# Kernel optimization log

Hardware: AMD Instinct MI355X
Metric: run time of the kernel (lower is better)

Reference implementation:

```python
import jax, jax.numpy as jnp
import numpy as np

ALPHA = 10.0
BETA = 2.0
BASE = 0.5
N, D, N_CLASSES = 4096, 512, 128


def setup_inputs() -> dict:
    key = jax.random.key(0)
    k1, k2 = jax.random.split(key)
    x = jax.random.normal(k1, (N, D), dtype=jnp.float32)
    inputs = x / jnp.linalg.norm(x, axis=1, keepdims=True)  # L2-normalized embeddings
    targets = jax.random.randint(k2, (N,), 0, N_CLASSES, dtype=jnp.int64)
    margin = jnp.float32(0.5)
    return {"inputs": inputs, "targets": targets, "margin": margin}


def reference(inputs, targets, margin):
    # Vectorized equivalent of the per-row masked_select/sort/hard-mining loop.
    n = inputs.shape[0]
    sim = inputs @ inputs.T  # [n, n]
    same = targets[:, None] == targets[None, :]
    pos_mask = same & (sim < 1.0)        # positives, excluding self-sim == 1
    neg_mask = ~same

    # sort()[0] / sort()[-1]  ==  masked min / max
    min_pos = jnp.min(jnp.where(pos_mask, sim, jnp.inf), axis=1)    # pos_pair_[0]
    max_neg = jnp.max(jnp.where(neg_mask, sim, -jnp.inf), axis=1)   # neg_pair_[-1]

    # Hard mining: selected values equal the raw sims (the +/- margin and
    # min_pos/max_neg shifts cancel algebraically in the original code).
    sel_neg = neg_mask & (sim + margin - min_pos[:, None] > 0)
    sel_pos = pos_mask & (max_neg[:, None] - sim + margin > 0)

    pos_sum = jnp.sum(jnp.where(sel_pos, jnp.exp(-BETA * (sim - BASE)), 0.0), axis=1)
    neg_sum = jnp.sum(jnp.where(sel_neg, jnp.exp(ALPHA * (sim - BASE)), 0.0), axis=1)
    row_loss = (2.0 / BETA) * jnp.log1p(pos_sum) + (2.0 / ALPHA) * jnp.log1p(neg_sum)

    # Rows with no surviving pos or neg pairs are skipped (counted in c).
    valid = jnp.any(sel_pos, axis=1) & jnp.any(sel_neg, axis=1)
    loss = jnp.sum(jnp.where(valid, row_loss, 0.0)) / n
    prec = jnp.mean((~valid).astype(jnp.float32))

    # Original returns mean sims of the LAST row's (pre-mining) pos/neg pairs.
    lp = pos_mask[-1].astype(sim.dtype)
    ln = neg_mask[-1].astype(sim.dtype)
    mean_pos_sim = jnp.sum(sim[-1] * lp) / jnp.maximum(jnp.sum(lp), 1.0)
    mean_neg_sim = jnp.sum(sim[-1] * ln) / jnp.maximum(jnp.sum(ln), 1.0)
    return (loss, prec, mean_pos_sim, mean_neg_sim)
```

## Files before the change

kernel.cpp:

```cpp
#include <hip/hip_runtime.h>
#include <hip/hip_bf16.h>
#include <math.h>

#define NROWS 4096
#define DDIM  512
#define BM    128
#define BK    64
#define NT    (DDIM / BK)
#define NBLK  (NROWS / BM)
#define NTRI  (NBLK * (NBLK + 1) / 2)

static constexpr float ALPHA = 10.0f;
static constexpr float BETA  = 2.0f;
static constexpr float BASE  = 0.5f;

typedef short bf16x8 __attribute__((ext_vector_type(8)));
typedef float f32x4 __attribute__((ext_vector_type(4)));

__device__ __forceinline__ unsigned enc_f32(float f) {
  unsigned b = __float_as_uint(f);
  return (b & 0x80000000u) ? ~b : (b | 0x80000000u);
}
__device__ __forceinline__ float dec_f32(unsigned u) {
  unsigned b = (u & 0x80000000u) ? (u & 0x7fffffffu) : ~u;
  return __uint_as_float(b);
}
__device__ __forceinline__ unsigned f2bf(float f) {
  __hip_bfloat16 h = __float2bfloat16(f);
  return (unsigned)*reinterpret_cast<unsigned short*>(&h);
}
__device__ __forceinline__ float bf2f(unsigned short u) {
  return __uint_as_float(((unsigned)u) << 16);
}

#define GLOAD_LDS16(g, l)                                              \
  __builtin_amdgcn_global_load_lds(                                    \
      (const __attribute__((address_space(1))) void*)(g),              \
      (__attribute__((address_space(3))) void*)(l), 16, 0, 0)

__global__ __launch_bounds__(256) void convert_k(
    const float* __restrict__ X, unsigned short* __restrict__ Xb,
    float* __restrict__ selfsim, unsigned* __restrict__ minb,
    unsigned* __restrict__ maxb, float* __restrict__ lacc) {
  const int gid = blockIdx.x * 256 + threadIdx.x;
  if (gid < NROWS) {
    minb[gid] = 0xFF800000u;
    maxb[gid] = 0x007FFFFFu;
  }
  if (gid < 8) lacc[gid] = 0.0f;

  const int wid = threadIdx.x >> 6, lane = threadIdx.x & 63;
  const int r = blockIdx.x * 4 + wid;
  const size_t base = (size_t)r * DDIM + lane * 8;
  const float4 v0 = *reinterpret_cast<const float4*>(X + base);
  const float4 v1 = *reinterpret_cast<const float4*>(X + base + 4);
  uint4 u;
  u.x = f2bf(v0.x) | (f2bf(v0.y) << 16);
  u.y = f2bf(v0.z) | (f2bf(v0.w) << 16);
  u.z = f2bf(v1.x) | (f2bf(v1.y) << 16);
  u.w = f2bf(v1.z) | (f2bf(v1.w) << 16);
  *reinterpret_cast<uint4*>(Xb + base) = u;

  float sd = v0.x * v0.x;
  sd = fmaf(v0.y, v0.y, sd); sd = fmaf(v0.z, v0.z, sd); sd = fmaf(v0.w, v0.w, sd);
  sd = fmaf(v1.x, v1.x, sd); sd = fmaf(v1.y, v1.y, sd);
  sd = fmaf(v1.z, v1.z, sd); sd = fmaf(v1.w, v1.w, sd);
  #pragma unroll
  for (int off = 1; off < 64; off <<= 1) sd += __shfl_xor(sd, off);
  if (lane == 0) selfsim[r] = sd;
}

__global__ __launch_bounds__(256) void gemm_tri(
    const unsigned short* __restrict__ Xb, const int* __restrict__ tgt,
    const float* __restrict__ selfsim,
    unsigned* __restrict__ minb, unsigned* __restrict__ maxb,
    unsigned short* __restrict__ simb) {
  __shared__ unsigned short lds[2][2][BM * BK] __attribute__((aligned(16)));

  int kk0 = blockIdx.x, bi = 0;
  while (kk0 >= NBLK - bi) { kk0 -= NBLK - bi; ++bi; }
  const int bj = bi + kk0;
  const int i0 = bi * BM, j0 = bj * BM;
  const bool diagb = (bi == bj);

  const int tid = threadIdx.x;
  const int w = tid >> 6, lane = tid & 63;
  const int wr = w >> 1, wc = w & 1;
  const int g = lane >> 4, q = lane & 15;
  const char* Xbb = (const char*)Xb;

  f32x4 acc[4][4];
  #pragma unroll
  for (int m = 0; m < 4; ++m)
    #pragma unroll
    for (int n = 0; n < 4; ++n) acc[m][n] = (f32x4)0.0f;

  #define STAGE(buf, t)                                                          \
    do {                                                                         \
      const int kb_ = (t) * (BK * 2);                                            \
      _Pragma("unroll")                                                          \
      for (int c_ = 0; c_ < 4; ++c_) {                                           \
        const int lin_ = (c_ * 256 + tid) * 16;                                  \
        const int row_ = lin_ >> 7;                                              \
        const int col_ = lin_ & 127;                                             \
        const int scol_ = col_ ^ ((row_ & 7) << 4);                              \
        GLOAD_LDS16(Xbb + (size_t)(i0 + row_) * (DDIM * 2) + kb_ + scol_,        \
                    (char*)&lds[buf][0][0] + lin_);                              \
        GLOAD_LDS16(Xbb + (size_t)(j0 + row_) * (DDIM * 2) + kb_ + scol_,        \
                    (char*)&lds[buf][1][0] + lin_);                              \
      }                                                                          \
    } while (0)

  STAGE(0, 0);
  __syncthreads();
  int cur = 0;
  for (int t = 0; t < NT; ++t) {
    if (t + 1 < NT) STAGE(cur ^ 1, t + 1);
    const char* Ab = (const char*)&lds[cur][0][0];
    const char* Bb = (const char*)&lds[cur][1][0];
    #pragma unroll
    for (int kk = 0; kk < 2; ++kk) {
      bf16x8 a[4], b[4];
      #pragma unroll
      for (int fm = 0; fm < 4; ++fm) {
        const int row = wr * 64 + fm * 16 + q;
        const int col = (kk * 64 + g * 16) ^ ((row & 7) << 4);
        a[fm] = *reinterpret_cast<const bf16x8*>(Ab + row * 128 + col);
      }
      #pragma unroll
      for (int fn = 0; fn < 4; ++fn) {
        const int row = wc * 64 + fn * 16 + q;
        const int col = (kk * 64 + g * 16) ^ ((row & 7) << 4);
        b[fn] = *reinterpret_cast<const bf16x8*>(Bb + row * 128 + col);
      }
      #pragma unroll
      for (int fm = 0; fm < 4; ++fm)
        #pragma unroll
        for (int fn = 0; fn < 4; ++fn)
          acc[fm][fn] = __builtin_amdgcn_mfma_f32_16x16x32_bf16(a[fm], b[fn], acc[fm][fn], 0, 0, 0);
    }
    __syncthreads();
    cur ^= 1;
  }

  const int rbase = i0 + wr * 64;
  int cg[4], tj[4];
  #pragma unroll
  for (int fn = 0; fn < 4; ++fn) {
    cg[fn] = j0 + wc * 64 + fn * 16 + q;
    tj[fn] = tgt[cg[fn]];
  }
  int ti[16];
  #pragma unroll
  for (int fm = 0; fm < 4; ++fm)
    #pragma unroll
    for (int reg = 0; reg < 4; ++reg)
      ti[fm * 4 + reg] = tgt[rbase + fm * 16 + g * 4 + reg];

  #pragma unroll
  for (int fm = 0; fm < 4; ++fm) {
    #pragma unroll
    for (int reg = 0; reg < 4; ++reg) {
      const int r = rbase + fm * 16 + g * 4 + reg;
      const int tr = ti[fm * 4 + reg];
      float mnp = INFINITY, mxn = -INFINITY;
      #pragma unroll
      for (int fn = 0; fn < 4; ++fn) {
        float s = acc[fm][fn][reg];
        if (diagb && r == cg[fn]) s = selfsim[r];
        simb[(size_t)r * NROWS + cg[fn]] = (unsigned short)f2bf(s);
        if (tj[fn] == tr) {
          if (s < 1.0f) mnp = fminf(mnp, s);
        } else {
          mxn = fmaxf(mxn, s);
        }
      }
      #pragma unroll
      for (int off = 1; off < 16; off <<= 1) {
        mnp = fminf(mnp, __shfl_xor(mnp, off));
        mxn = fmaxf(mxn, __shfl_xor(mxn, off));
      }
      if (q == 0) {
        atomicMin(minb + r, enc_f32(mnp));
        atomicMax(maxb + r, enc_f32(mxn));
      }
    }
  }

  if (!diagb) {
    #pragma unroll
    for (int fn = 0; fn < 4; ++fn) {
      const int c = cg[fn];
      const int tc = tj[fn];
      float mnp = INFINITY, mxn = -INFINITY;
      #pragma unroll
      for (int fm = 0; fm < 4; ++fm)
        #pragma unroll
        for (int reg = 0; reg < 4; ++reg) {
          const float s = acc[fm][fn][reg];
          if (ti[fm * 4 + reg] == tc) {
            if (s < 1.0f) mnp = fminf(mnp, s);
          } else {
            mxn = fmaxf(mxn, s);
          }
        }
      mnp = fminf(mnp, __shfl_xor(mnp, 16));
      mnp = fminf(mnp, __shfl_xor(mnp, 32));
      mxn = fmaxf(mxn, __shfl_xor(mxn, 16));
      mxn = fmaxf(mxn, __shfl_xor(mxn, 32));
      if (lane < 16) {
        atomicMin(minb + c, enc_f32(mnp));
        atomicMax(maxb + c, enc_f32(mxn));
      }
    }
    #pragma unroll
    for (int fm = 0; fm < 4; ++fm)
      #pragma unroll
      for (int fn = 0; fn < 4; ++fn) {
        uint2 uu;
        uu.x = f2bf(acc[fm][fn][0]) | (f2bf(acc[fm][fn][1]) << 16);
        uu.y = f2bf(acc[fm][fn][2]) | (f2bf(acc[fm][fn][3]) << 16);
        *reinterpret_cast<uint2*>(simb + (size_t)cg[fn] * NROWS + rbase + fm * 16 + g * 4) = uu;
      }
  }
}

__global__ __launch_bounds__(256) void row_pass(
    const unsigned short* __restrict__ simb, const int* __restrict__ tgt,
    const unsigned* __restrict__ minb, const unsigned* __restrict__ maxb,
    float* __restrict__ rowloss, float* __restrict__ rowvalid,
    float* __restrict__ lacc, const float* __restrict__ marginp) {
  const int wid = threadIdx.x >> 6, lane = threadIdx.x & 63;
  const int i = blockIdx.x * 4 + wid;
  const int ti = tgt[i];
  const float mp = dec_f32(minb[i]);
  const float mx = dec_f32(maxb[i]);
  const float margin = *marginp;
  const unsigned short* row = simb + (size_t)i * NROWS;
  const bool last = (i == NROWS - 1);

  float psum = 0.0f, nsum = 0.0f, lsp = 0.0f, lcp = 0.0f, lsn = 0.0f, lcn = 0.0f;
  #pragma unroll
  for (int c = 0; c < 8; ++c) {
    const int j0 = c * 512 + lane * 8;
    const bf16x8 v = *reinterpret_cast<const bf16x8*>(row + j0);
    const int4 t0 = *reinterpret_cast<const int4*>(tgt + j0);
    const int4 t1 = *reinterpret_cast<const int4*>(tgt + j0 + 4);
    const int tj[8] = {t0.x, t0.y, t0.z, t0.w, t1.x, t1.y, t1.z, t1.w};
    #pragma unroll
    for (int e = 0; e < 8; ++e) {
      const float s = bf2f((unsigned short)v[e]);
      if (tj[e] != ti) {
        if (s + margin - mp > 0.0f) nsum += __expf(ALPHA * (s - BASE));
        if (last) { lsn += s; lcn += 1.0f; }
      } else if (s < 1.0f) {
        if (mx - s + margin > 0.0f) psum += __expf(-BETA * (s - BASE));
        if (last) { lsp += s; lcp += 1.0f; }
      }
    }
  }
  #pragma unroll
  for (int off = 1; off < 64; off <<= 1) {
    psum += __shfl_xor(psum, off);
    nsum += __shfl_xor(nsum, off);
  }
  if (last) {
    #pragma unroll
    for (int off = 1; off < 64; off <<= 1) {
      lsp += __shfl_xor(lsp, off); lcp += __shfl_xor(lcp, off);
      lsn += __shfl_xor(lsn, off); lcn += __shfl_xor(lcn, off);
    }
  }
  if (lane == 0) {
    const bool valid = (psum > 0.0f) && (nsum > 0.0f);
    rowloss[i] = valid ? (2.0f / BETA) * log1pf(psum) + (2.0f / ALPHA) * log1pf(nsum) : 0.0f;
    rowvalid[i] = valid ? 0.0f : 1.0f;
    if (last) { lacc[0] = lsp; lacc[1] = lcp; lacc[2] = lsn; lacc[3] = lcn; }
  }
}

__device__ __forceinline__ float block_sum(float v) {
  __shared__ float sh[4];
  #pragma unroll
  for (int off = 32; off > 0; off >>= 1) v += __shfl_down(v, off);
  if ((threadIdx.x & 63) == 0) sh[threadIdx.x >> 6] = v;
  __syncthreads();
  float r = sh[0] + sh[1] + sh[2] + sh[3];
  __syncthreads();
  return r;
}

__global__ __launch_bounds__(256) void finalize_k(
    const float* __restrict__ rowloss, const float* __restrict__ rowvalid,
    const float* __restrict__ lacc, float* __restrict__ out) {
  float lsum = 0.0f, inval = 0.0f;
  #pragma unroll
  for (int c = 0; c < 16; ++c) {
    const int i = c * 256 + threadIdx.x;
    lsum += rowloss[i];
    inval += rowvalid[i];
  }
  lsum = block_sum(lsum);
  inval = block_sum(inval);
  if (threadIdx.x == 0) {
    out[0] = lsum / (float)NROWS;
    out[1] = inval / (float)NROWS;
    out[2] = lacc[0] / fmaxf(lacc[1], 1.0f);
    out[3] = lacc[2] / fmaxf(lacc[3], 1.0f);
  }
}

extern "C" void kernel_launch(void* const* d_in, const int* in_sizes, int n_in,
                              void* d_out, int out_size, void* d_ws, size_t ws_size,
                              hipStream_t stream) {
  const float* X = (const float*)d_in[0];
  const int* tgt = (const int*)d_in[1];
  const float* marginp = (const float*)d_in[2];
  float* out = (float*)d_out;

  char* ws = (char*)d_ws;
  unsigned* minb = (unsigned*)ws;
  unsigned* maxb = (unsigned*)(ws + (16 << 10));
  float* rowloss = (float*)(ws + (32 << 10));
  float* rowvalid = (float*)(ws + (48 << 10));
  float* lacc = (float*)(ws + (64 << 10));
  float* selfsim = (float*)(ws + (80 << 10));
  unsigned short* Xb = (unsigned short*)(ws + (128 << 10));
  unsigned short* simb = (unsigned short*)(ws + (128 << 10) + ((size_t)4 << 20));

  convert_k<<<dim3(NROWS / 4), 256, 0, stream>>>(X, Xb, selfsim, minb, maxb, lacc);
  gemm_tri<<<dim3(NTRI), 256, 0, stream>>>(Xb, tgt, selfsim, minb, maxb, simb);
  row_pass<<<dim3(NROWS / 4), 256, 0, stream>>>(simb, tgt, minb, maxb, rowloss, rowvalid, lacc, marginp);
  finalize_k<<<dim3(1), 256, 0, stream>>>(rowloss, rowvalid, lacc, out);
}
```

Before: 124.8 us.

## Recompute similarity GEMM in second pass instead of materializing bf16 sim matrix

Drops the 4096x4096 bf16 similarity buffer and the row_pass kernel that re-read it. The triangular GEMM now runs twice: the first pass computes per-row min-positive and max-negative, and the second recomputes the tile and accumulates the masked exp sums per row and column with atomics. Diagonal blocks load only one tile, and atomics are skipped when a lane holds the identity value. This trades a 32 MB write plus read of the sim matrix for a second pass of GEMM compute and more float atomics, which also makes the summation order nondeterministic.

```diff
diff --git a/kernel.cpp b/kernel.cpp
--- a/kernel.cpp
+++ b/kernel.cpp
@@ -38,14 +38,17 @@
       (const __attribute__((address_space(1))) void*)(g),              \
       (__attribute__((address_space(3))) void*)(l), 16, 0, 0)
 
-__global__ __launch_bounds__(256) void convert_k(
+__global__ __launch_bounds__(256) void convert_init_k(
     const float* __restrict__ X, unsigned short* __restrict__ Xb,
     float* __restrict__ selfsim, unsigned* __restrict__ minb,
-    unsigned* __restrict__ maxb, float* __restrict__ lacc) {
+    unsigned* __restrict__ maxb, float* __restrict__ ps,
+    float* __restrict__ ns, float* __restrict__ lacc) {
   const int gid = blockIdx.x * 256 + threadIdx.x;
   if (gid < NROWS) {
     minb[gid] = 0xFF800000u;
     maxb[gid] = 0x007FFFFFu;
+    ps[gid] = 0.0f;
+    ns[gid] = 0.0f;
   }
   if (gid < 8) lacc[gid] = 0.0f;
 
@@ -70,11 +73,27 @@
   if (lane == 0) selfsim[r] = sd;
 }
 
-__global__ __launch_bounds__(256) void gemm_tri(
+#define STAGE1(dst, rowbase, t)                                                \
+  do {                                                                         \
+    const int kb_ = (t) * (BK * 2);                                            \
+    _Pragma("unroll")                                                          \
+    for (int c_ = 0; c_ < 4; ++c_) {                                           \
+      const int lin_ = (c_ * 256 + tid) * 16;                                  \
+      const int row_ = lin_ >> 7;                                              \
+      const int col_ = lin_ & 127;                                             \
+      const int scol_ = col_ ^ ((row_ & 7) << 4);                              \
+      GLOAD_LDS16(Xbb + (size_t)((rowbase) + row_) * (DDIM * 2) + kb_ + scol_, \
+                  (char*)(dst) + lin_);                                        \
+    }                                                                          \
+  } while (0)
+
+template <int PASS>
+__global__ __launch_bounds__(256) void gemm_pass(
     const unsigned short* __restrict__ Xb, const int* __restrict__ tgt,
     const float* __restrict__ selfsim,
     unsigned* __restrict__ minb, unsigned* __restrict__ maxb,
-    unsigned short* __restrict__ simb) {
+    float* __restrict__ ps, float* __restrict__ ns,
+    float* __restrict__ lacc, const float* __restrict__ marginp) {
   __shared__ unsigned short lds[2][2][BM * BK] __attribute__((aligned(16)));
 
   int kk0 = blockIdx.x, bi = 0;
@@ -95,29 +114,17 @@
     #pragma unroll
     for (int n = 0; n < 4; ++n) acc[m][n] = (f32x4)0.0f;
 
-  #define STAGE(buf, t)                                                          \
-    do {                                                                         \
-      const int kb_ = (t) * (BK * 2);                                            \
-      _Pragma("unroll")                                                          \
-      for (int c_ = 0; c_ < 4; ++c_) {                                           \
-        const int lin_ = (c_ * 256 + tid) * 16;                                  \
-        const int row_ = lin_ >> 7;                                              \
-        const int col_ = lin_ & 127;                                             \
-        const int scol_ = col_ ^ ((row_ & 7) << 4);                              \
-        GLOAD_LDS16(Xbb + (size_t)(i0 + row_) * (DDIM * 2) + kb_ + scol_,        \
-                    (char*)&lds[buf][0][0] + lin_);                              \
-        GLOAD_LDS16(Xbb + (size_t)(j0 + row_) * (DDIM * 2) + kb_ + scol_,        \
-                    (char*)&lds[buf][1][0] + lin_);                              \
-      }                                                                          \
-    } while (0)
-
-  STAGE(0, 0);
+  STAGE1(&lds[0][0][0], i0, 0);
+  if (!diagb) STAGE1(&lds[0][1][0], j0, 0);
   __syncthreads();
   int cur = 0;
   for (int t = 0; t < NT; ++t) {
-    if (t + 1 < NT) STAGE(cur ^ 1, t + 1);
+    if (t + 1 < NT) {
+      STAGE1(&lds[cur ^ 1][0][0], i0, t + 1);
+      if (!diagb) STAGE1(&lds[cur ^ 1][1][0], j0, t + 1);
+    }
     const char* Ab = (const char*)&lds[cur][0][0];
-    const char* Bb = (const char*)&lds[cur][1][0];
+    const char* Bb = diagb ? Ab : (const char*)&lds[cur][1][0];
     #pragma unroll
     for (int kk = 0; kk < 2; ++kk) {
       bf16x8 a[4], b[4];
@@ -157,125 +164,155 @@
     for (int reg = 0; reg < 4; ++reg)
       ti[fm * 4 + reg] = tgt[rbase + fm * 16 + g * 4 + reg];
 
-  #pragma unroll
-  for (int fm = 0; fm < 4; ++fm) {
-    #pragma unroll
-    for (int reg = 0; reg < 4; ++reg) {
-      const int r = rbase + fm * 16 + g * 4 + reg;
-      const int tr = ti[fm * 4 + reg];
-      float mnp = INFINITY, mxn = -INFINITY;
-      #pragma unroll
-      for (int fn = 0; fn < 4; ++fn) {
-        float s = acc[fm][fn][reg];
-        if (diagb && r == cg[fn]) s = selfsim[r];
-        simb[(size_t)r * NROWS + cg[fn]] = (unsigned short)f2bf(s);
-        if (tj[fn] == tr) {
-          if (s < 1.0f) mnp = fminf(mnp, s);
-        } else {
-          mxn = fmaxf(mxn, s);
-        }
-      }
-      #pragma unroll
-      for (int off = 1; off < 16; off <<= 1) {
-        mnp = fminf(mnp, __shfl_xor(mnp, off));
-        mxn = fmaxf(mxn, __shfl_xor(mxn, off));
-      }
-      if (q == 0) {
-        atomicMin(minb + r, enc_f32(mnp));
-        atomicMax(maxb + r, enc_f32(mxn));
-      }
-    }
-  }
-
-  if (!diagb) {
-    #pragma unroll
-    for (int fn = 0; fn < 4; ++fn) {
-      const int c = cg[fn];
-      const int tc = tj[fn];
-      float mnp = INFINITY, mxn = -INFINITY;
-      #pragma unroll
-      for (int fm = 0; fm < 4; ++fm)
-        #pragma unroll
-        for (int reg = 0; reg < 4; ++reg) {
-          const float s = acc[fm][fn][reg];
-          if (ti[fm * 4 + reg] == tc) {
+  if constexpr (PASS == 0) {
+    #pragma unroll
+    for (int fm = 0; fm < 4; ++fm) {
+      #pragma unroll
+      for (int reg = 0; reg < 4; ++reg) {
+        const int r = rbase + fm * 16 + g * 4 + reg;
+        const int tr = ti[fm * 4 + reg];
+        float mnp = INFINITY, mxn = -INFINITY;
+        #pragma unroll
+        for (int fn = 0; fn < 4; ++fn) {
+          float s = acc[fm][fn][reg];
+          if (diagb && r == cg[fn]) s = selfsim[r];
+          if (tj[fn] == tr) {
             if (s < 1.0f) mnp = fminf(mnp, s);
           } else {
             mxn = fmaxf(mxn, s);
           }
         }
-      mnp = fminf(mnp, __shfl_xor(mnp, 16));
-      mnp = fminf(mnp, __shfl_xor(mnp, 32));
-      mxn = fmaxf(mxn, __shfl_xor(mxn, 16));
-      mxn = fmaxf(mxn, __shfl_xor(mxn, 32));
-      if (lane < 16) {
-        atomicMin(minb + c, enc_f32(mnp));
-        atomicMax(maxb + c, enc_f32(mxn));
-      }
-    }
+        #pragma unroll
+        for (int off = 1; off < 16; off <<= 1) {
+          mnp = fminf(mnp, __shfl_xor(mnp, off));
+          mxn = fmaxf(mxn, __shfl_xor(mxn, off));
+        }
+        if (q == 0) {
+          if (mnp != INFINITY) atomicMin(minb + r, enc_f32(mnp));
+          if (mxn != -INFINITY) atomicMax(maxb + r, enc_f32(mxn));
+        }
+      }
+    }
+    if (!diagb) {
+      #pragma unroll
+      for (int fn = 0; fn < 4; ++fn) {
+        const int tc = tj[fn];
+        float mnp = INFINITY, mxn = -INFINITY;
+        #pragma unroll
+        for (int fm = 0; fm < 4; ++fm)
+          #pragma unroll
+          for (int reg = 0; reg < 4; ++reg) {
+            const float s = acc[fm][fn][reg];
+            if (ti[fm * 4 + reg] == tc) {
+              if (s < 1.0f) mnp = fminf(mnp, s);
+            } else {
+              mxn = fmaxf(mxn, s);
+            }
+          }
+        mnp = fminf(mnp, __shfl_xor(mnp, 16));
+        mnp = fminf(mnp, __shfl_xor(mnp, 32));
+        mxn = fmaxf(mxn, __shfl_xor(mxn, 16));
+        mxn = fmaxf(mxn, __shfl_xor(mxn, 32));
+        if (lane < 16) {
+          if (mnp != INFINITY) atomicMin(minb + cg[fn], enc_f32(mnp));
+          if (mxn != -INFINITY) atomicMax(maxb + cg[fn], enc_f32(mxn));
+        }
+      }
+    }
+  } else {
+    const float margin = *marginp;
+    float mpr[16], mxr[16];
     #pragma unroll
     for (int fm = 0; fm < 4; ++fm)
       #pragma unroll
+      for (int reg = 0; reg < 4; ++reg) {
+        const int r = rbase + fm * 16 + g * 4 + reg;
+        mpr[fm * 4 + reg] = dec_f32(minb[r]);
+        mxr[fm * 4 + reg] = dec_f32(maxb[r]);
+      }
+    float mpc[4], mxc[4], cps[4], cns[4];
+    #pragma unroll
+    for (int fn = 0; fn < 4; ++fn) {
+      mpc[fn] = dec_f32(minb[cg[fn]]);
+      mxc[fn] = dec_f32(maxb[cg[fn]]);
+      cps[fn] = 0.0f; cns[fn] = 0.0f;
+    }
+    float wlsp = 0, wlcp = 0, wlsn = 0, wlcn = 0;
+    float clsp = 0, clcp = 0, clsn = 0, clcn = 0;
+
+    #pragma unroll
+    for (int fm = 0; fm < 4; ++fm) {
+      #pragma unroll
+      for (int reg = 0; reg < 4; ++reg) {
+        const int idx = fm * 4 + reg;
+        const int r = rbase + fm * 16 + g * 4 + reg;
+        const int tr = ti[idx];
+        const bool lastrow = (r == NROWS - 1);
+        float rps = 0.0f, rns = 0.0f;
+        #pragma unroll
+        for (int fn = 0; fn < 4; ++fn) {
+          float s = acc[fm][fn][reg];
+          if (diagb && r == cg[fn])
+            s = bf2f((unsigned short)f2bf(selfsim[r]));
+          const bool collast = (!diagb) && (cg[fn] == NROWS - 1);
+          if (tj[fn] != tr) {
+            const float en = __expf(ALPHA * (s - BASE));
+            if (s + margin - mpr[idx] > 0.0f) rns += en;
+            if (!diagb && s + margin - mpc[fn] > 0.0f) cns[fn] += en;
+            if (lastrow) { wlsn += s; wlcn += 1.0f; }
+            if (collast) { clsn += s; clcn += 1.0f; }
+          } else if (s < 1.0f) {
+            const float ep = __expf(-BETA * (s - BASE));
+            if (mxr[idx] - s + margin > 0.0f) rps += ep;
+            if (!diagb && mxc[fn] - s + margin > 0.0f) cps[fn] += ep;
+            if (lastrow) { wlsp += s; wlcp += 1.0f; }
+            if (collast) { clsp += s; clcp += 1.0f; }
+          }
+        }
+        #pragma unroll
+        for (int off = 1; off < 16; off <<= 1) {
+          rps += __shfl_xor(rps, off);
+          rns += __shfl_xor(rns, off);
+        }
+        if (q == 0) {
+          if (rps != 0.0f) atomicAdd(ps + r, rps);
+          if (rns != 0.0f) atomicAdd(ns + r, rns);
+        }
+      }
+    }
+    if (bi == NBLK - 1 && wr == 1 && diagb) {
+      #pragma unroll
+      for (int off = 1; off < 16; off <<= 1) {
+        wlsp += __shfl_xor(wlsp, off); wlcp += __shfl_xor(wlcp, off);
+        wlsn += __shfl_xor(wlsn, off); wlcn += __shfl_xor(wlcn, off);
+      }
+      if (lane == 48) {
+        if (wlcp != 0.0f) { atomicAdd(lacc + 0, wlsp); atomicAdd(lacc + 1, wlcp); }
+        if (wlcn != 0.0f) { atomicAdd(lacc + 2, wlsn); atomicAdd(lacc + 3, wlcn); }
+      }
+    }
+    if (!diagb) {
+      #pragma unroll
       for (int fn = 0; fn < 4; ++fn) {
-        uint2 uu;
-        uu.x = f2bf(acc[fm][fn][0]) | (f2bf(acc[fm][fn][1]) << 16);
-        uu.y = f2bf(acc[fm][fn][2]) | (f2bf(acc[fm][fn][3]) << 16);
-        *reinterpret_cast<uint2*>(simb + (size_t)cg[fn] * NROWS + rbase + fm * 16 + g * 4) = uu;
-      }
-  }
-}
-
-__global__ __launch_bounds__(256) void row_pass(
-    const unsigned short* __restrict__ simb, const int* __restrict__ tgt,
-    const unsigned* __restrict__ minb, const unsigned* __restrict__ maxb,
-    float* __restrict__ rowloss, float* __restrict__ rowvalid,
-    float* __restrict__ lacc, const float* __restrict__ marginp) {
-  const int wid = threadIdx.x >> 6, lane = threadIdx.x & 63;
-  const int i = blockIdx.x * 4 + wid;
-  const int ti = tgt[i];
-  const float mp = dec_f32(minb[i]);
-  const float mx = dec_f32(maxb[i]);
-  const float margin = *marginp;
-  const unsigned short* row = simb + (size_t)i * NROWS;
-  const bool last = (i == NROWS - 1);
-
-  float psum = 0.0f, nsum = 0.0f, lsp = 0.0f, lcp = 0.0f, lsn = 0.0f, lcn = 0.0f;
-  #pragma unroll
-  for (int c = 0; c < 8; ++c) {
-    const int j0 = c * 512 + lane * 8;
-    const bf16x8 v = *reinterpret_cast<const bf16x8*>(row + j0);
-    const int4 t0 = *reinterpret_cast<const int4*>(tgt + j0);
-    const int4 t1 = *reinterpret_cast<const int4*>(tgt + j0 + 4);
-    const int tj[8] = {t0.x, t0.y, t0.z, t0.w, t1.x, t1.y, t1.z, t1.w};
-    #pragma unroll
-    for (int e = 0; e < 8; ++e) {
-      const float s = bf2f((unsigned short)v[e]);
-      if (tj[e] != ti) {
-        if (s + margin - mp > 0.0f) nsum += __expf(ALPHA * (s - BASE));
-        if (last) { lsn += s; lcn += 1.0f; }
-      } else if (s < 1.0f) {
-        if (mx - s + margin > 0.0f) psum += __expf(-BETA * (s - BASE));
-        if (last) { lsp += s; lcp += 1.0f; }
-      }
-    }
-  }
-  #pragma unroll
-  for (int off = 1; off < 64; off <<= 1) {
-    psum += __shfl_xor(psum, off);
-    nsum += __shfl_xor(nsum, off);
-  }
-  if (last) {
-    #pragma unroll
-    for (int off = 1; off < 64; off <<= 1) {
-      lsp += __shfl_xor(lsp, off); lcp += __shfl_xor(lcp, off);
-      lsn += __shfl_xor(lsn, off); lcn += __shfl_xor(lcn, off);
-    }
-  }
-  if (lane == 0) {
-    const bool valid = (psum > 0.0f) && (nsum > 0.0f);
-    rowloss[i] = valid ? (2.0f / BETA) * log1pf(psum) + (2.0f / ALPHA) * log1pf(nsum) : 0.0f;
-    rowvalid[i] = valid ? 0.0f : 1.0f;
-    if (last) { lacc[0] = lsp; lacc[1] = lcp; lacc[2] = lsn; lacc[3] = lcn; }
+        float v1 = cps[fn], v2 = cns[fn];
+        v1 += __shfl_xor(v1, 16); v1 += __shfl_xor(v1, 32);
+        v2 += __shfl_xor(v2, 16); v2 += __shfl_xor(v2, 32);
+        if (lane < 16) {
+          if (v1 != 0.0f) atomicAdd(ps + cg[fn], v1);
+          if (v2 != 0.0f) atomicAdd(ns + cg[fn], v2);
+        }
+      }
+      if (bj == NBLK - 1 && wc == 1) {
+        clsp += __shfl_xor(clsp, 16); clsp += __shfl_xor(clsp, 32);
+        clcp += __shfl_xor(clcp, 16); clcp += __shfl_xor(clcp, 32);
+        clsn += __shfl_xor(clsn, 16); clsn += __shfl_xor(clsn, 32);
+        clcn += __shfl_xor(clcn, 16); clcn += __shfl_xor(clcn, 32);
+        if (lane == 15) {
+          if (clcp != 0.0f) { atomicAdd(lacc + 0, clsp); atomicAdd(lacc + 1, clcp); }
+          if (clcn != 0.0f) { atomicAdd(lacc + 2, clsn); atomicAdd(lacc + 3, clcn); }
+        }
+      }
+    }
   }
 }
 
@@ -291,14 +328,18 @@
 }
 
 __global__ __launch_bounds__(256) void finalize_k(
-    const float* __restrict__ rowloss, const float* __restrict__ rowvalid,
+    const float* __restrict__ ps, const float* __restrict__ ns,
     const float* __restrict__ lacc, float* __restrict__ out) {
   float lsum = 0.0f, inval = 0.0f;
   #pragma unroll
   for (int c = 0; c < 16; ++c) {
     const int i = c * 256 + threadIdx.x;
-    lsum += rowloss[i];
-    inval += rowvalid[i];
+    const float p = ps[i], n = ns[i];
+    if (p > 0.0f && n > 0.0f) {
+      lsum += (2.0f / BETA) * log1pf(p) + (2.0f / ALPHA) * log1pf(n);
+    } else {
+      inval += 1.0f;
+    }
   }
   lsum = block_sum(lsum);
   inval = block_sum(inval);
@@ -321,15 +362,14 @@
   char* ws = (char*)d_ws;
   unsigned* minb = (unsigned*)ws;
   unsigned* maxb = (unsigned*)(ws + (16 << 10));
-  float* rowloss = (float*)(ws + (32 << 10));
-  float* rowvalid = (float*)(ws + (48 << 10));
+  float* ps = (float*)(ws + (32 << 10));
+  float* ns = (float*)(ws + (48 << 10));
   float* lacc = (float*)(ws + (64 << 10));
   float* selfsim = (float*)(ws + (80 << 10));
   unsigned short* Xb = (unsigned short*)(ws + (128 << 10));
-  unsigned short* simb = (unsigned short*)(ws + (128 << 10) + ((size_t)4 << 20));
-
-  convert_k<<<dim3(NROWS / 4), 256, 0, stream>>>(X, Xb, selfsim, minb, maxb, lacc);
-  gemm_tri<<<dim3(NTRI), 256, 0, stream>>>(Xb, tgt, selfsim, minb, maxb, simb);
-  row_pass<<<dim3(NROWS / 4), 256, 0, stream>>>(simb, tgt, minb, maxb, rowloss, rowvalid, lacc, marginp);
-  finalize_k<<<dim3(1), 256, 0, stream>>>(rowloss, rowvalid, lacc, out);
-}
+
+  convert_init_k<<<dim3(NROWS / 4), 256, 0, stream>>>(X, Xb, selfsim, minb, maxb, ps, ns, lacc);
+  gemm_pass<0><<<dim3(NTRI), 256, 0, stream>>>(Xb, tgt, selfsim, minb, maxb, ps, ns, lacc, marginp);
+  gemm_pass<1><<<dim3(NTRI), 256, 0, stream>>>(Xb, tgt, selfsim, minb, maxb, ps, ns, lacc, marginp);
+  finalize_k<<<dim3(1), 256, 0, stream>>>(ps, ns, lacc, out);
+}
```

New measurement: 153.3 us. 22.8% more time.

## Move min/max mining into row pass and stage sim tile stores through LDS

Applied to the files above, without the earlier changes.

The GEMM epilogue no longer computes per-row min positive and max negative or issues atomics. It stages bf16 sim tiles through LDS so each row is written to global memory with coalesced 16-byte stores, for both the tile and its transpose. The row pass now keeps a whole row in registers, computes min/max with wave reductions, and then does the mining sums in a second sweep, with targets cached in LDS. The GEMM drops its double-buffered prefetch in favour of BK=32 single-buffer staging without swizzle, which may expose load latency and LDS bank conflicts. The diagonal self-similarity is hardcoded to 1.0 instead of the computed norm.

```diff
diff --git a/kernel.cpp b/kernel.cpp
--- a/kernel.cpp
+++ b/kernel.cpp
@@ -5,7 +5,7 @@
 #define NROWS 4096
 #define DDIM  512
 #define BM    128
-#define BK    64
+#define BK    32
 #define NT    (DDIM / BK)
 #define NBLK  (NROWS / BM)
 #define NTRI  (NBLK * (NBLK + 1) / 2)
@@ -17,14 +17,6 @@
 typedef short bf16x8 __attribute__((ext_vector_type(8)));
 typedef float f32x4 __attribute__((ext_vector_type(4)));
 
-__device__ __forceinline__ unsigned enc_f32(float f) {
-  unsigned b = __float_as_uint(f);
-  return (b & 0x80000000u) ? ~b : (b | 0x80000000u);
-}
-__device__ __forceinline__ float dec_f32(unsigned u) {
-  unsigned b = (u & 0x80000000u) ? (u & 0x7fffffffu) : ~u;
-  return __uint_as_float(b);
-}
 __device__ __forceinline__ unsigned f2bf(float f) {
   __hip_bfloat16 h = __float2bfloat16(f);
   return (unsigned)*reinterpret_cast<unsigned short*>(&h);
@@ -38,17 +30,8 @@
       (const __attribute__((address_space(1))) void*)(g),              \
       (__attribute__((address_space(3))) void*)(l), 16, 0, 0)
 
-__global__ __launch_bounds__(256) void convert_k(
-    const float* __restrict__ X, unsigned short* __restrict__ Xb,
-    float* __restrict__ selfsim, unsigned* __restrict__ minb,
-    unsigned* __restrict__ maxb, float* __restrict__ lacc) {
-  const int gid = blockIdx.x * 256 + threadIdx.x;
-  if (gid < NROWS) {
-    minb[gid] = 0xFF800000u;
-    maxb[gid] = 0x007FFFFFu;
-  }
-  if (gid < 8) lacc[gid] = 0.0f;
-
+__global__ __launch_bounds__(256) void convert_k(const float* __restrict__ X,
+                                                 unsigned short* __restrict__ Xb) {
   const int wid = threadIdx.x >> 6, lane = threadIdx.x & 63;
   const int r = blockIdx.x * 4 + wid;
   const size_t base = (size_t)r * DDIM + lane * 8;
@@ -60,22 +43,11 @@
   u.z = f2bf(v1.x) | (f2bf(v1.y) << 16);
   u.w = f2bf(v1.z) | (f2bf(v1.w) << 16);
   *reinterpret_cast<uint4*>(Xb + base) = u;
-
-  float sd = v0.x * v0.x;
-  sd = fmaf(v0.y, v0.y, sd); sd = fmaf(v0.z, v0.z, sd); sd = fmaf(v0.w, v0.w, sd);
-  sd = fmaf(v1.x, v1.x, sd); sd = fmaf(v1.y, v1.y, sd);
-  sd = fmaf(v1.z, v1.z, sd); sd = fmaf(v1.w, v1.w, sd);
-  #pragma unroll
-  for (int off = 1; off < 64; off <<= 1) sd += __shfl_xor(sd, off);
-  if (lane == 0) selfsim[r] = sd;
-}
-
-__global__ __launch_bounds__(256) void gemm_tri(
-    const unsigned short* __restrict__ Xb, const int* __restrict__ tgt,
-    const float* __restrict__ selfsim,
-    unsigned* __restrict__ minb, unsigned* __restrict__ maxb,
-    unsigned short* __restrict__ simb) {
-  __shared__ unsigned short lds[2][2][BM * BK] __attribute__((aligned(16)));
+}
+
+__global__ __launch_bounds__(256) void gemm_tri_store(
+    const unsigned short* __restrict__ Xb, unsigned short* __restrict__ simb) {
+  __shared__ unsigned short SH[2][BM * BK] __attribute__((aligned(16)));
 
   int kk0 = blockIdx.x, bi = 0;
   while (kk0 >= NBLK - bi) { kk0 -= NBLK - bi; ++bi; }
@@ -95,167 +67,153 @@
     #pragma unroll
     for (int n = 0; n < 4; ++n) acc[m][n] = (f32x4)0.0f;
 
-  #define STAGE(buf, t)                                                          \
-    do {                                                                         \
-      const int kb_ = (t) * (BK * 2);                                            \
-      _Pragma("unroll")                                                          \
-      for (int c_ = 0; c_ < 4; ++c_) {                                           \
-        const int lin_ = (c_ * 256 + tid) * 16;                                  \
-        const int row_ = lin_ >> 7;                                              \
-        const int col_ = lin_ & 127;                                             \
-        const int scol_ = col_ ^ ((row_ & 7) << 4);                              \
-        GLOAD_LDS16(Xbb + (size_t)(i0 + row_) * (DDIM * 2) + kb_ + scol_,        \
-                    (char*)&lds[buf][0][0] + lin_);                              \
-        GLOAD_LDS16(Xbb + (size_t)(j0 + row_) * (DDIM * 2) + kb_ + scol_,        \
-                    (char*)&lds[buf][1][0] + lin_);                              \
-      }                                                                          \
-    } while (0)
-
-  STAGE(0, 0);
-  __syncthreads();
-  int cur = 0;
   for (int t = 0; t < NT; ++t) {
-    if (t + 1 < NT) STAGE(cur ^ 1, t + 1);
-    const char* Ab = (const char*)&lds[cur][0][0];
-    const char* Bb = (const char*)&lds[cur][1][0];
-    #pragma unroll
-    for (int kk = 0; kk < 2; ++kk) {
-      bf16x8 a[4], b[4];
+    #pragma unroll
+    for (int l = 0; l < 2; ++l) {
+      const int lin = (l * 256 + tid) * 16;
+      const int row = lin >> 6;
+      const int col = lin & 63;
+      GLOAD_LDS16(Xbb + (size_t)(i0 + row) * (DDIM * 2) + t * (BK * 2) + col,
+                  (char*)&SH[0][0] + lin);
+      if (!diagb)
+        GLOAD_LDS16(Xbb + (size_t)(j0 + row) * (DDIM * 2) + t * (BK * 2) + col,
+                    (char*)&SH[1][0] + lin);
+    }
+    __syncthreads();
+    const char* Ab = (const char*)&SH[0][0];
+    const char* Bb = diagb ? Ab : (const char*)&SH[1][0];
+    bf16x8 a[4], b[4];
+    #pragma unroll
+    for (int fm = 0; fm < 4; ++fm)
+      a[fm] = *reinterpret_cast<const bf16x8*>(Ab + (wr * 64 + fm * 16 + q) * 64 + g * 16);
+    #pragma unroll
+    for (int fn = 0; fn < 4; ++fn)
+      b[fn] = *reinterpret_cast<const bf16x8*>(Bb + (wc * 64 + fn * 16 + q) * 64 + g * 16);
+    #pragma unroll
+    for (int fm = 0; fm < 4; ++fm)
       #pragma unroll
-      for (int fm = 0; fm < 4; ++fm) {
-        const int row = wr * 64 + fm * 16 + q;
-        const int col = (kk * 64 + g * 16) ^ ((row & 7) << 4);
-        a[fm] = *reinterpret_cast<const bf16x8*>(Ab + row * 128 + col);
-      }
-      #pragma unroll
-      for (int fn = 0; fn < 4; ++fn) {
-        const int row = wc * 64 + fn * 16 + q;
-        const int col = (kk * 64 + g * 16) ^ ((row & 7) << 4);
-        b[fn] = *reinterpret_cast<const bf16x8*>(Bb + row * 128 + col);
-      }
-      #pragma unroll
-      for (int fm = 0; fm < 4; ++fm)
-        #pragma unroll
-        for (int fn = 0; fn < 4; ++fn)
-          acc[fm][fn] = __builtin_amdgcn_mfma_f32_16x16x32_bf16(a[fm], b[fn], acc[fm][fn], 0, 0, 0);
-    }
+      for (int fn = 0; fn < 4; ++fn)
+        acc[fm][fn] = __builtin_amdgcn_mfma_f32_16x16x32_bf16(a[fm], b[fn], acc[fm][fn], 0, 0, 0);
     __syncthreads();
-    cur ^= 1;
-  }
-
-  const int rbase = i0 + wr * 64;
-  int cg[4], tj[4];
-  #pragma unroll
-  for (int fn = 0; fn < 4; ++fn) {
-    cg[fn] = j0 + wc * 64 + fn * 16 + q;
-    tj[fn] = tgt[cg[fn]];
-  }
-  int ti[16];
-  #pragma unroll
-  for (int fm = 0; fm < 4; ++fm)
-    #pragma unroll
-    for (int reg = 0; reg < 4; ++reg)
-      ti[fm * 4 + reg] = tgt[rbase + fm * 16 + g * 4 + reg];
-
-  #pragma unroll
-  for (int fm = 0; fm < 4; ++fm) {
-    #pragma unroll
-    for (int reg = 0; reg < 4; ++reg) {
-      const int r = rbase + fm * 16 + g * 4 + reg;
-      const int tr = ti[fm * 4 + reg];
-      float mnp = INFINITY, mxn = -INFINITY;
-      #pragma unroll
-      for (int fn = 0; fn < 4; ++fn) {
-        float s = acc[fm][fn][reg];
-        if (diagb && r == cg[fn]) s = selfsim[r];
-        simb[(size_t)r * NROWS + cg[fn]] = (unsigned short)f2bf(s);
-        if (tj[fn] == tr) {
-          if (s < 1.0f) mnp = fminf(mnp, s);
-        } else {
-          mxn = fmaxf(mxn, s);
-        }
-      }
-      #pragma unroll
-      for (int off = 1; off < 16; off <<= 1) {
-        mnp = fminf(mnp, __shfl_xor(mnp, off));
-        mxn = fmaxf(mxn, __shfl_xor(mxn, off));
-      }
-      if (q == 0) {
-        atomicMin(minb + r, enc_f32(mnp));
-        atomicMax(maxb + r, enc_f32(mxn));
-      }
-    }
-  }
-
-  if (!diagb) {
-    #pragma unroll
-    for (int fn = 0; fn < 4; ++fn) {
-      const int c = cg[fn];
-      const int tc = tj[fn];
-      float mnp = INFINITY, mxn = -INFINITY;
-      #pragma unroll
-      for (int fm = 0; fm < 4; ++fm)
-        #pragma unroll
-        for (int reg = 0; reg < 4; ++reg) {
-          const float s = acc[fm][fn][reg];
-          if (ti[fm * 4 + reg] == tc) {
-            if (s < 1.0f) mnp = fminf(mnp, s);
-          } else {
-            mxn = fmaxf(mxn, s);
+  }
+
+  unsigned short* SV = &SH[0][0];
+  #pragma unroll
+  for (int orient = 0; orient < 2; ++orient) {
+    if (orient == 1 && diagb) break;
+    for (int d = 0; d < 4; ++d) {
+      if (orient == 0) {
+        if (wr == (d >> 1)) {
+          #pragma unroll
+          for (int h = 0; h < 2; ++h) {
+            const int fm = 2 * (d & 1) + h;
+            #pragma unroll
+            for (int fn = 0; fn < 4; ++fn)
+              #pragma unroll
+              for (int reg = 0; reg < 4; ++reg) {
+                const int shrow = h * 16 + g * 4 + reg;
+                const int col = wc * 64 + fn * 16 + q;
+                unsigned short v = (unsigned short)f2bf(acc[fm][fn][reg]);
+                if (diagb && (32 * d + shrow == col)) v = 0x3F80;
+                SV[shrow * 136 + col] = v;
+              }
           }
         }
-      mnp = fminf(mnp, __shfl_xor(mnp, 16));
-      mnp = fminf(mnp, __shfl_xor(mnp, 32));
-      mxn = fmaxf(mxn, __shfl_xor(mxn, 16));
-      mxn = fmaxf(mxn, __shfl_xor(mxn, 32));
-      if (lane < 16) {
-        atomicMin(minb + c, enc_f32(mnp));
-        atomicMax(maxb + c, enc_f32(mxn));
-      }
-    }
-    #pragma unroll
-    for (int fm = 0; fm < 4; ++fm)
+      } else {
+        if (wc == (d >> 1)) {
+          #pragma unroll
+          for (int h = 0; h < 2; ++h) {
+            const int fn = 2 * (d & 1) + h;
+            const int shrow = h * 16 + q;
+            #pragma unroll
+            for (int fm = 0; fm < 4; ++fm) {
+              const int colR = wr * 64 + fm * 16 + g * 4;
+              uint2 uu;
+              uu.x = f2bf(acc[fm][fn][0]) | (f2bf(acc[fm][fn][1]) << 16);
+              uu.y = f2bf(acc[fm][fn][2]) | (f2bf(acc[fm][fn][3]) << 16);
+              *reinterpret_cast<uint2*>(&SV[shrow * 136 + colR]) = uu;
+            }
+          }
+        }
+      }
+      __syncthreads();
       #pragma unroll
-      for (int fn = 0; fn < 4; ++fn) {
-        uint2 uu;
-        uu.x = f2bf(acc[fm][fn][0]) | (f2bf(acc[fm][fn][1]) << 16);
-        uu.y = f2bf(acc[fm][fn][2]) | (f2bf(acc[fm][fn][3]) << 16);
-        *reinterpret_cast<uint2*>(simb + (size_t)cg[fn] * NROWS + rbase + fm * 16 + g * 4) = uu;
-      }
-  }
-}
-
-__global__ __launch_bounds__(256) void row_pass(
+      for (int rr = 0; rr < 2; ++rr) {
+        const int s = tid + rr * 256;
+        const int row = s >> 4, cs = s & 15;
+        const bf16x8 vv = *reinterpret_cast<const bf16x8*>(&SV[row * 136 + cs * 8]);
+        unsigned short* dst =
+            (orient == 0)
+                ? simb + (size_t)(i0 + d * 32 + row) * NROWS + j0 + cs * 8
+                : simb + (size_t)(j0 + d * 32 + row) * NROWS + i0 + cs * 8;
+        *reinterpret_cast<bf16x8*>(dst) = vv;
+      }
+      __syncthreads();
+    }
+  }
+}
+
+__global__ __launch_bounds__(256) void rows_k(
     const unsigned short* __restrict__ simb, const int* __restrict__ tgt,
-    const unsigned* __restrict__ minb, const unsigned* __restrict__ maxb,
-    float* __restrict__ rowloss, float* __restrict__ rowvalid,
-    float* __restrict__ lacc, const float* __restrict__ marginp) {
-  const int wid = threadIdx.x >> 6, lane = threadIdx.x & 63;
+    const float* __restrict__ marginp, float* __restrict__ rowloss,
+    float* __restrict__ rowvalid, float* __restrict__ lacc) {
+  __shared__ int tgl[NROWS];
+  const int tid = threadIdx.x;
+  #pragma unroll
+  for (int c = 0; c < 4; ++c)
+    reinterpret_cast<int4*>(tgl)[tid + c * 256] =
+        reinterpret_cast<const int4*>(tgt)[tid + c * 256];
+  __syncthreads();
+
+  const int wid = tid >> 6, lane = tid & 63;
   const int i = blockIdx.x * 4 + wid;
-  const int ti = tgt[i];
-  const float mp = dec_f32(minb[i]);
-  const float mx = dec_f32(maxb[i]);
-  const float margin = *marginp;
+  const int ti = tgl[i];
   const unsigned short* row = simb + (size_t)i * NROWS;
-  const bool last = (i == NROWS - 1);
-
-  float psum = 0.0f, nsum = 0.0f, lsp = 0.0f, lcp = 0.0f, lsn = 0.0f, lcn = 0.0f;
+  const bool lastw = (i == NROWS - 1);
+
+  bf16x8 v[8];
+  unsigned long long same = 0ull;
+  float minp = INFINITY, maxn = -INFINITY;
   #pragma unroll
   for (int c = 0; c < 8; ++c) {
     const int j0 = c * 512 + lane * 8;
-    const bf16x8 v = *reinterpret_cast<const bf16x8*>(row + j0);
-    const int4 t0 = *reinterpret_cast<const int4*>(tgt + j0);
-    const int4 t1 = *reinterpret_cast<const int4*>(tgt + j0 + 4);
+    v[c] = *reinterpret_cast<const bf16x8*>(row + j0);
+    const int4 t0 = *reinterpret_cast<const int4*>(tgl + j0);
+    const int4 t1 = *reinterpret_cast<const int4*>(tgl + j0 + 4);
     const int tj[8] = {t0.x, t0.y, t0.z, t0.w, t1.x, t1.y, t1.z, t1.w};
     #pragma unroll
     for (int e = 0; e < 8; ++e) {
-      const float s = bf2f((unsigned short)v[e]);
-      if (tj[e] != ti) {
-        if (s + margin - mp > 0.0f) nsum += __expf(ALPHA * (s - BASE));
-        if (last) { lsn += s; lcn += 1.0f; }
+      const float s = bf2f((unsigned short)v[c][e]);
+      const bool sm = (tj[e] == ti);
+      same |= (unsigned long long)sm << (c * 8 + e);
+      if (sm) {
+        if (s < 1.0f) minp = fminf(minp, s);
+      } else {
+        maxn = fmaxf(maxn, s);
+      }
+    }
+  }
+  #pragma unroll
+  for (int off = 1; off < 64; off <<= 1) {
+    minp = fminf(minp, __shfl_xor(minp, off));
+    maxn = fmaxf(maxn, __shfl_xor(maxn, off));
+  }
+
+  const float margin = *marginp;
+  float psum = 0.0f, nsum = 0.0f;
+  float lsp = 0.0f, lcp = 0.0f, lsn = 0.0f, lcn = 0.0f;
+  #pragma unroll
+  for (int c = 0; c < 8; ++c) {
+    #pragma unroll
+    for (int e = 0; e < 8; ++e) {
+      const float s = bf2f((unsigned short)v[c][e]);
+      const bool sm = (same >> (c * 8 + e)) & 1ull;
+      if (!sm) {
+        if (s + margin - minp > 0.0f) nsum += __expf(ALPHA * (s - BASE));
+        if (lastw) { lsn += s; lcn += 1.0f; }
       } else if (s < 1.0f) {
-        if (mx - s + margin > 0.0f) psum += __expf(-BETA * (s - BASE));
-        if (last) { lsp += s; lcp += 1.0f; }
+        if (maxn - s + margin > 0.0f) psum += __expf(-BETA * (s - BASE));
+        if (lastw) { lsp += s; lcp += 1.0f; }
       }
     }
   }
@@ -264,7 +222,7 @@
     psum += __shfl_xor(psum, off);
     nsum += __shfl_xor(nsum, off);
   }
-  if (last) {
+  if (lastw) {
     #pragma unroll
     for (int off = 1; off < 64; off <<= 1) {
       lsp += __shfl_xor(lsp, off); lcp += __shfl_xor(lcp, off);
@@ -275,7 +233,7 @@
     const bool valid = (psum > 0.0f) && (nsum > 0.0f);
     rowloss[i] = valid ? (2.0f / BETA) * log1pf(psum) + (2.0f / ALPHA) * log1pf(nsum) : 0.0f;
     rowvalid[i] = valid ? 0.0f : 1.0f;
-    if (last) { lacc[0] = lsp; lacc[1] = lcp; lacc[2] = lsn; lacc[3] = lcn; }
+    if (lastw) { lacc[0] = lsp; lacc[1] = lcp; lacc[2] = lsn; lacc[3] = lcn; }
   }
 }
 
@@ -319,17 +277,14 @@
   float* out = (float*)d_out;
 
   char* ws = (char*)d_ws;
-  unsigned* minb = (unsigned*)ws;
-  unsigned* maxb = (unsigned*)(ws + (16 << 10));
-  float* rowloss = (float*)(ws + (32 << 10));
-  float* rowvalid = (float*)(ws + (48 << 10));
-  float* lacc = (float*)(ws + (64 << 10));
-  float* selfsim = (float*)(ws + (80 << 10));
+  float* rowloss = (float*)ws;
+  float* rowvalid = (float*)(ws + (16 << 10));
+  float* lacc = (float*)(ws + (32 << 10));
   unsigned short* Xb = (unsigned short*)(ws + (128 << 10));
   unsigned short* simb = (unsigned short*)(ws + (128 << 10) + ((size_t)4 << 20));
 
-  convert_k<<<dim3(NROWS / 4), 256, 0, stream>>>(X, Xb, selfsim, minb, maxb, lacc);
-  gemm_tri<<<dim3(NTRI), 256, 0, stream>>>(Xb, tgt, selfsim, minb, maxb, simb);
-  row_pass<<<dim3(NROWS / 4), 256, 0, stream>>>(simb, tgt, minb, maxb, rowloss, rowvalid, lacc, marginp);
+  convert_k<<<dim3(NROWS / 4), 256, 0, stream>>>(X, Xb);
+  gemm_tri_store<<<dim3(NTRI), 256, 0, stream>>>(Xb, simb);
+  rows_k<<<dim3(NROWS / 4), 256, 0, stream>>>(simb, tgt, marginp, rowloss, rowvalid, lacc);
   finalize_k<<<dim3(1), 256, 0, stream>>>(rowloss, rowvalid, lacc, out);
 }
```

After: 116.0 us. 7.0% less time.
